# Performance work log

Measured on AMD Instinct MI355X. Metric: run time of the kernel, lower is better.

## Reference

```python
import jax, jax.numpy as jnp
import numpy as np

B, H, W, C = 8, 64, 64, 256
RC = C // 8  # reduced channels per build()

def setup_inputs() -> dict:
    key = jax.random.key(0)
    ks = jax.random.split(key, 4)
    x = jax.random.normal(ks[0], (B, H, W, C), dtype=jnp.float32)
    # 1x1 conv kernels flattened to [Cin, Cout]; glorot-ish scale
    wq = jax.random.normal(ks[1], (C, RC), dtype=jnp.float32) * (1.0 / np.sqrt(C))
    wk = jax.random.normal(ks[2], (C, RC), dtype=jnp.float32) * (1.0 / np.sqrt(C))
    wv = jax.random.normal(ks[3], (C, C), dtype=jnp.float32) * (1.0 / np.sqrt(C))
    bq = jnp.zeros((RC,), dtype=jnp.float32)
    bk = jnp.zeros((RC,), dtype=jnp.float32)
    bv = jnp.zeros((C,), dtype=jnp.float32)
    return {"x": x, "wq": wq, "bq": bq, "wk": wk, "bk": bk, "wv": wv, "bv": bv}

def reference(x, wq, bq, wk, bk, wv, bv):
    b, h, w, c = x.shape
    n = h * w
    # 1x1 convs == per-pixel channel matmuls; q/k have relu activation, v does not
    q = jax.nn.relu(jnp.einsum('bhwc,cd->bhwd', x, wq) + bq).reshape(b, n, -1)  # [B,N,RC]
    k = jax.nn.relu(jnp.einsum('bhwc,cd->bhwd', x, wk) + bk).reshape(b, n, -1)  # [B,N,RC]
    v = (jnp.einsum('bhwc,cd->bhwd', x, wv) + bv).reshape(b, n, c)              # [B,N,C]
    attn = jax.nn.softmax(jnp.einsum('bnd,bmd->bnm', q, k), axis=-1)            # [B,N,N]
    out = jnp.einsum('bnm,bmc->bnc', attn, v).reshape(b, h, w, c)
    return out + x
```

## Files before the change

kernel.cpp:

```cpp
#include <hip/hip_runtime.h>
#include <hip/hip_bf16.h>

typedef __attribute__((ext_vector_type(8))) short s16x8;
typedef __attribute__((ext_vector_type(4))) float f32x4;
typedef __attribute__((ext_vector_type(4))) unsigned int u32x4;

#define BATCH 8
#define NPIX  4096
#define CCH   256
#define RCH   32
#define TK    32
#define HALFK 2048
#define NIT   (HALFK / TK)
#define THR   8.0f
#define LOG2E 1.4426950408889634f

__device__ __forceinline__ unsigned short f2bf(float f) {
  __hip_bfloat16 h = __float2bfloat16(f);
  return __builtin_bit_cast(unsigned short, h);
}

__device__ __forceinline__ unsigned int cvt_pk(float lo, float hi) {
  unsigned int r;
  asm("v_cvt_pk_bf16_f32 %0, %1, %2" : "=v"(r) : "v"(lo), "v"(hi));
  return r;
}

__device__ __forceinline__ void gload_lds16(const void* g, void* l) {
  __builtin_amdgcn_global_load_lds(
      (const __attribute__((address_space(1))) void*)g,
      (__attribute__((address_space(3))) void*)l, 16, 0, 0);
}

__global__ void prep_kernel(const float* __restrict__ x,
                            const float* __restrict__ wq,
                            const float* __restrict__ wk,
                            const float* __restrict__ wv,
                            unsigned short* __restrict__ xb,
                            unsigned short* __restrict__ wqkT,
                            unsigned short* __restrict__ wvT) {
  int stride = gridDim.x * blockDim.x;
  int i0 = blockIdx.x * blockDim.x + threadIdx.x;
  const int nx4 = BATCH * NPIX * CCH / 4;
  for (int i = i0; i < nx4; i += stride) {
    float4 v = reinterpret_cast<const float4*>(x)[i];
    ushort4 o;
    o.x = f2bf(v.x); o.y = f2bf(v.y); o.z = f2bf(v.z); o.w = f2bf(v.w);
    reinterpret_cast<ushort4*>(xb)[i] = o;
  }
  for (int i = i0; i < 64 * CCH; i += stride) {
    int d = i >> 8, c = i & 255;
    float v = (d < RCH) ? wq[c * RCH + d] : wk[c * RCH + (d - RCH)];
    wqkT[i] = f2bf(v);
  }
  for (int i = i0; i < CCH * CCH; i += stride) {
    int d = i >> 8, c = i & 255;
    wvT[i] = f2bf(wv[c * CCH + d]);
  }
}

__global__ void proj_kernel(const unsigned short* __restrict__ xb,
                            const unsigned short* __restrict__ wqkT,
                            const unsigned short* __restrict__ wvT,
                            const float* __restrict__ bq,
                            const float* __restrict__ bk,
                            const float* __restrict__ bv,
                            unsigned short* __restrict__ qb,
                            unsigned short* __restrict__ kb,
                            unsigned short* __restrict__ vT) {
  int t = threadIdx.x;
  int w = t >> 6, l = t & 63, g = l >> 4, lc = l & 15;
  f32x4 zero = {0.f, 0.f, 0.f, 0.f};

  if (blockIdx.x < 512) {
    int row0 = blockIdx.x * 64 + w * 16;
    f32x4 acc[4];
    for (int ct = 0; ct < 4; ++ct) acc[ct] = zero;
    for (int ks = 0; ks < 8; ++ks) {
      s16x8 a = *reinterpret_cast<const s16x8*>(
          xb + (size_t)(row0 + lc) * CCH + ks * 32 + g * 8);
      for (int ct = 0; ct < 4; ++ct) {
        s16x8 bfr = *reinterpret_cast<const s16x8*>(
            wqkT + (size_t)(ct * 16 + lc) * CCH + ks * 32 + g * 8);
        acc[ct] = __builtin_amdgcn_mfma_f32_16x16x32_bf16(a, bfr, acc[ct], 0, 0, 0);
      }
    }
    for (int ct = 0; ct < 4; ++ct) {
      int col = ct * 16 + lc;
      float bias = (col < RCH) ? bq[col] : bk[col - RCH];
      for (int r = 0; r < 4; ++r) {
        int row = row0 + 4 * g + r;
        float v = fmaxf(acc[ct][r] + bias, 0.f);
        if (col < RCH) qb[(size_t)row * RCH + col] = f2bf(v * LOG2E);
        else           kb[(size_t)row * RCH + (col - RCH)] = f2bf(v);
      }
    }
  } else {
    int idx = blockIdx.x - 512;
    int b = idx & 7; idx >>= 3;
    int dt = idx & 3; int nt = idx >> 2;
    int d0 = dt * 64 + w * 16;
    int n0 = nt * 64;
    f32x4 acc[4];
    for (int ct = 0; ct < 4; ++ct) acc[ct] = zero;
    for (int ks = 0; ks < 8; ++ks) {
      s16x8 a = *reinterpret_cast<const s16x8*>(
          wvT + (size_t)(d0 + lc) * CCH + ks * 32 + g * 8);
      for (int ct = 0; ct < 4; ++ct) {
        s16x8 bfr = *reinterpret_cast<const s16x8*>(
            xb + ((size_t)b * NPIX + n0 + ct * 16 + lc) * CCH + ks * 32 + g * 8);
        acc[ct] = __builtin_amdgcn_mfma_f32_16x16x32_bf16(a, bfr, acc[ct], 0, 0, 0);
      }
    }
    for (int ct = 0; ct < 4; ++ct) {
      for (int r = 0; r < 4; ++r) {
        int d = d0 + 4 * g + r;
        int n = n0 + ct * 16 + lc;
        vT[((size_t)b * CCH + d) * NPIX + n] = f2bf(acc[ct][r] + bv[d]);
      }
    }
  }
}

__global__ __launch_bounds__(256, 2)
void attn_kernel(const unsigned short* __restrict__ qb,
                 const unsigned short* __restrict__ kb,
                 const unsigned short* __restrict__ vT,
                 const float* __restrict__ x,
                 float* __restrict__ out) {
  __shared__ __attribute__((aligned(16))) unsigned short Vlds[2][CCH * 64];
  __shared__ __attribute__((aligned(16))) float mergeLS[2][32];
  __shared__ float mLds[2];

  int b  = blockIdx.x & 7;
  int qt = blockIdx.x >> 3;
  int t  = threadIdx.x;
  int w = t >> 6, l = t & 63, g = l >> 4, lc = l & 15;
  int a = w >> 1, s = w & 1;
  const size_t bN = (size_t)b * NPIX;
  f32x4 zero = {0.f, 0.f, 0.f, 0.f};

  const unsigned short* kbase = kb + bN * RCH;
  const unsigned short* vbase = vT + (size_t)b * CCH * NPIX;

  int qbase = qt * 64 + a * 32;
  s16x8 qfA = *reinterpret_cast<const s16x8*>(qb + (bN + qbase + lc) * RCH + g * 8);
  s16x8 qfB = *reinterpret_cast<const s16x8*>(qb + (bN + qbase + 16 + lc) * RCH + g * 8);

  int chb = t >> 3, gr = t & 7;
  int gsw = gr ^ (chb & 7);
  int koff = (gsw < 4) ? (gsw * 8) : (HALFK + (gsw - 4) * 8);
  const unsigned short* vsrc = vbase + (size_t)chb * NPIX + koff;

  int krb = 8 * (lc >> 2) + (lc & 3);
  int kO  = s * HALFK + krb;

  unsigned int swz = (lc & 7) << 4;
  int vrS = (s * 64 + g * 16) ^ swz;

  s16x8 ones;
  #pragma unroll
  for (int i = 0; i < 8; ++i) ones[i] = (short)0x3F80;

  f32x4 o[2][16];
  #pragma unroll
  for (int qh = 0; qh < 2; ++qh)
    #pragma unroll
    for (int cc = 0; cc < 16; ++cc) o[qh][cc] = zero;
  f32x4 ols[2];
  ols[0] = zero; ols[1] = zero;
  float m = -1e30f;

  #pragma unroll
  for (int i = 0; i < 8; ++i)
    gload_lds16(vsrc + (size_t)i * 32 * NPIX,
                (char*)&Vlds[0][0] + i * 4096 + t * 16);
  s16x8 kf0 = *reinterpret_cast<const s16x8*>(kbase + (size_t)(kO + 0) * RCH + g * 8);
  s16x8 kf1 = *reinterpret_cast<const s16x8*>(kbase + (size_t)(kO + 4) * RCH + g * 8);
  __syncthreads();

  for (int it = 0; it < NIT; ++it) {
    int p = it & 1;
    int kv = it * TK;
    bool nx = (it + 1) < NIT;

    if (nx) {
      #pragma unroll
      for (int i = 0; i < 8; ++i)
        gload_lds16(vsrc + kv + TK + (size_t)i * 32 * NPIX,
                    (char*)&Vlds[p ^ 1][0] + i * 4096 + t * 16);
    }

    f32x4 sA0 = __builtin_amdgcn_mfma_f32_16x16x32_bf16(kf0, qfA, zero, 0, 0, 0);
    f32x4 sA1 = __builtin_amdgcn_mfma_f32_16x16x32_bf16(kf1, qfA, zero, 0, 0, 0);
    f32x4 sB0 = __builtin_amdgcn_mfma_f32_16x16x32_bf16(kf0, qfB, zero, 0, 0, 0);
    f32x4 sB1 = __builtin_amdgcn_mfma_f32_16x16x32_bf16(kf1, qfB, zero, 0, 0, 0);

    if (nx) {
      kf0 = *reinterpret_cast<const s16x8*>(
          kbase + (size_t)(kO + kv + TK + 0) * RCH + g * 8);
      kf1 = *reinterpret_cast<const s16x8*>(
          kbase + (size_t)(kO + kv + TK + 4) * RCH + g * 8);
    }

    float xA = fmaxf(fmaxf(sA0[0], sA0[1]), fmaxf(sA0[2], sA0[3]));
    float xB = fmaxf(fmaxf(sA1[0], sA1[1]), fmaxf(sA1[2], sA1[3]));
    float xC = fmaxf(fmaxf(sB0[0], sB0[1]), fmaxf(sB0[2], sB0[3]));
    float xD = fmaxf(fmaxf(sB1[0], sB1[1]), fmaxf(sB1[2], sB1[3]));
    float pmax = fmaxf(fmaxf(xA, xB), fmaxf(xC, xD));

    float sc = 1.f;
    int resc = !__all(pmax - m <= THR);
    if (resc) {
      #pragma unroll
      for (int off = 1; off <= 32; off <<= 1)
        pmax = fmaxf(pmax, __shfl_xor(pmax, off));
      float mnew = fmaxf(m, pmax);
      sc = exp2f(m - mnew);
      m = mnew;
    }

    unsigned int pkA[4], pkB[4];
    pkA[0] = cvt_pk(exp2f(sA0[0] - m), exp2f(sA0[1] - m));
    pkA[1] = cvt_pk(exp2f(sA0[2] - m), exp2f(sA0[3] - m));
    pkA[2] = cvt_pk(exp2f(sA1[0] - m), exp2f(sA1[1] - m));
    pkA[3] = cvt_pk(exp2f(sA1[2] - m), exp2f(sA1[3] - m));
    pkB[0] = cvt_pk(exp2f(sB0[0] - m), exp2f(sB0[1] - m));
    pkB[1] = cvt_pk(exp2f(sB0[2] - m), exp2f(sB0[3] - m));
    pkB[2] = cvt_pk(exp2f(sB1[0] - m), exp2f(sB1[1] - m));
    pkB[3] = cvt_pk(exp2f(sB1[2] - m), exp2f(sB1[3] - m));

    if (resc) {
      #pragma unroll
      for (int qh = 0; qh < 2; ++qh) {
        #pragma unroll
        for (int cc = 0; cc < 16; ++cc)
          #pragma unroll
          for (int r = 0; r < 4; ++r) o[qh][cc][r] *= sc;
        #pragma unroll
        for (int r = 0; r < 4; ++r) ols[qh][r] *= sc;
      }
    }

    u32x4 uA = {pkA[0], pkA[1], pkA[2], pkA[3]};
    u32x4 uB = {pkB[0], pkB[1], pkB[2], pkB[3]};
    s16x8 paA = __builtin_bit_cast(s16x8, uA);
    s16x8 paB = __builtin_bit_cast(s16x8, uB);
    const char* pb = (const char*)&Vlds[p][0] + lc * 128 + vrS;
    __builtin_amdgcn_s_setprio(1);
    ols[0] = __builtin_amdgcn_mfma_f32_16x16x32_bf16(paA, ones, ols[0], 0, 0, 0);
    ols[1] = __builtin_amdgcn_mfma_f32_16x16x32_bf16(paB, ones, ols[1], 0, 0, 0);
    #pragma unroll
    for (int cc = 0; cc < 16; ++cc) {
      s16x8 vb = *reinterpret_cast<const s16x8*>(pb + cc * 2048);
      o[0][cc] = __builtin_amdgcn_mfma_f32_16x16x32_bf16(paA, vb, o[0][cc], 0, 0, 0);
      o[1][cc] = __builtin_amdgcn_mfma_f32_16x16x32_bf16(paB, vb, o[1][cc], 0, 0, 0);
    }
    __builtin_amdgcn_s_setprio(0);

    __syncthreads();
  }

  if (s == 1) {
    if (lc == 0) {
      *reinterpret_cast<f32x4*>(&mergeLS[a][4 * g])      = ols[0];
      *reinterpret_cast<f32x4*>(&mergeLS[a][16 + 4 * g]) = ols[1];
    }
    if (l == 0) mLds[a] = m;
  }
  __syncthreads();

  float* mrg = (float*)&Vlds[0][0];
  if (s == 1) {
    float* base = mrg + a * 8192 + l * 128;
    #pragma unroll
    for (int qh = 0; qh < 2; ++qh)
      #pragma unroll
      for (int cc = 0; cc < 16; ++cc) {
        int idx = qh * 16 + cc;
        *reinterpret_cast<f32x4*>(base + ((idx + l) & 31) * 4) = o[qh][cc];
      }
  }
  __syncthreads();
  if (s == 0) {
    float mB = mLds[a];
    float mT = fmaxf(m, mB);
    float sAc = exp2f(m - mT), sBc = exp2f(mB - mT);
    const float* base = mrg + a * 8192 + l * 128;
    #pragma unroll
    for (int qh = 0; qh < 2; ++qh) {
      f32x4 lB4 = *reinterpret_cast<const f32x4*>(&mergeLS[a][qh * 16 + 4 * g]);
      f32x4 rl;
      #pragma unroll
      for (int r = 0; r < 4; ++r)
        rl[r] = 1.0f / (ols[qh][r] * sAc + lB4[r] * sBc);
      #pragma unroll
      for (int cc = 0; cc < 16; ++cc) {
        int idx = qh * 16 + cc;
        f32x4 ob = *reinterpret_cast<const f32x4*>(base + ((idx + l) & 31) * 4);
        #pragma unroll
        for (int r = 0; r < 4; ++r) {
          size_t row = bN + qbase + qh * 16 + 4 * g + r;
          size_t oi = row * CCH + cc * 16 + lc;
          out[oi] = (o[qh][cc][r] * sAc + ob[r] * sBc) * rl[r] + x[oi];
        }
      }
    }
  }
}

extern "C" void kernel_launch(void* const* d_in, const int* in_sizes, int n_in,
                              void* d_out, int out_size, void* d_ws, size_t ws_size,
                              hipStream_t stream) {
  const float* x  = (const float*)d_in[0];
  const float* wq = (const float*)d_in[1];
  const float* bq = (const float*)d_in[2];
  const float* wk = (const float*)d_in[3];
  const float* bk = (const float*)d_in[4];
  const float* wv = (const float*)d_in[5];
  const float* bv = (const float*)d_in[6];
  float* out = (float*)d_out;

  unsigned short* ws   = (unsigned short*)d_ws;
  unsigned short* qb   = ws;
  unsigned short* kb   = qb + 1048576;
  unsigned short* vT   = kb + 1048576;
  unsigned short* xb   = vT + 8388608;
  unsigned short* wqkT = xb + 8388608;
  unsigned short* wvT  = wqkT + 16384;

  prep_kernel<<<dim3(2048), dim3(256), 0, stream>>>(x, wq, wk, wv, xb, wqkT, wvT);
  proj_kernel<<<dim3(2560), dim3(256), 0, stream>>>(xb, wqkT, wvT, bq, bk, bv,
                                                    qb, kb, vT);
  attn_kernel<<<dim3(512), dim3(256), 0, stream>>>(qb, kb, vT, x, out);
}
```

Before: 164.4 us.

## Fuse x bf16 conversion into projection kernel via padded LDS tile

Removes the full-tensor fp32-to-bf16 conversion pass over x and its bf16 workspace. Each projection block now loads its 64-row fp32 slice of x, converts it to bf16 into a padded shared-memory tile, and feeds the MFMA operands from LDS. Weight prep stays as a small separate kernel. The trade-off is that the value-projection blocks re-read fp32 x four times instead of bf16, doubling the bytes of that redundant traffic.

```diff
diff --git a/kernel.cpp b/kernel.cpp
--- a/kernel.cpp
+++ b/kernel.cpp
@@ -14,6 +14,7 @@
 #define NIT   (HALFK / TK)
 #define THR   8.0f
 #define LOG2E 1.4426950408889634f
+#define XPAD  264
 
 __device__ __forceinline__ unsigned short f2bf(float f) {
   __hip_bfloat16 h = __float2bfloat16(f);
@@ -32,22 +33,13 @@
       (__attribute__((address_space(3))) void*)l, 16, 0, 0);
 }
 
-__global__ void prep_kernel(const float* __restrict__ x,
-                            const float* __restrict__ wq,
-                            const float* __restrict__ wk,
-                            const float* __restrict__ wv,
-                            unsigned short* __restrict__ xb,
-                            unsigned short* __restrict__ wqkT,
-                            unsigned short* __restrict__ wvT) {
+__global__ void wprep_kernel(const float* __restrict__ wq,
+                             const float* __restrict__ wk,
+                             const float* __restrict__ wv,
+                             unsigned short* __restrict__ wqkT,
+                             unsigned short* __restrict__ wvT) {
   int stride = gridDim.x * blockDim.x;
   int i0 = blockIdx.x * blockDim.x + threadIdx.x;
-  const int nx4 = BATCH * NPIX * CCH / 4;
-  for (int i = i0; i < nx4; i += stride) {
-    float4 v = reinterpret_cast<const float4*>(x)[i];
-    ushort4 o;
-    o.x = f2bf(v.x); o.y = f2bf(v.y); o.z = f2bf(v.z); o.w = f2bf(v.w);
-    reinterpret_cast<ushort4*>(xb)[i] = o;
-  }
   for (int i = i0; i < 64 * CCH; i += stride) {
     int d = i >> 8, c = i & 255;
     float v = (d < RCH) ? wq[c * RCH + d] : wk[c * RCH + (d - RCH)];
@@ -59,26 +51,41 @@
   }
 }
 
-__global__ void proj_kernel(const unsigned short* __restrict__ xb,
-                            const unsigned short* __restrict__ wqkT,
-                            const unsigned short* __restrict__ wvT,
-                            const float* __restrict__ bq,
-                            const float* __restrict__ bk,
-                            const float* __restrict__ bv,
-                            unsigned short* __restrict__ qb,
-                            unsigned short* __restrict__ kb,
-                            unsigned short* __restrict__ vT) {
+__global__ __launch_bounds__(256)
+void proj_kernel(const float* __restrict__ x,
+                 const unsigned short* __restrict__ wqkT,
+                 const unsigned short* __restrict__ wvT,
+                 const float* __restrict__ bq,
+                 const float* __restrict__ bk,
+                 const float* __restrict__ bv,
+                 unsigned short* __restrict__ qb,
+                 unsigned short* __restrict__ kb,
+                 unsigned short* __restrict__ vT) {
+  __shared__ __attribute__((aligned(16))) unsigned short Xt[64 * XPAD];
+
   int t = threadIdx.x;
   int w = t >> 6, l = t & 63, g = l >> 4, lc = l & 15;
   f32x4 zero = {0.f, 0.f, 0.f, 0.f};
 
   if (blockIdx.x < 512) {
-    int row0 = blockIdx.x * 64 + w * 16;
+    int row0 = blockIdx.x * 64;
+    #pragma unroll
+    for (int i = 0; i < 16; ++i) {
+      int flat4 = i * 256 + t;
+      int row = flat4 >> 6, col4 = flat4 & 63;
+      float4 v = *reinterpret_cast<const float4*>(
+          x + ((size_t)(row0 + row)) * CCH + col4 * 4);
+      ushort4 o4;
+      o4.x = f2bf(v.x); o4.y = f2bf(v.y); o4.z = f2bf(v.z); o4.w = f2bf(v.w);
+      *reinterpret_cast<ushort4*>(&Xt[row * XPAD + col4 * 4]) = o4;
+    }
+    __syncthreads();
+
     f32x4 acc[4];
     for (int ct = 0; ct < 4; ++ct) acc[ct] = zero;
     for (int ks = 0; ks < 8; ++ks) {
       s16x8 a = *reinterpret_cast<const s16x8*>(
-          xb + (size_t)(row0 + lc) * CCH + ks * 32 + g * 8);
+          &Xt[(w * 16 + lc) * XPAD + ks * 32 + g * 8]);
       for (int ct = 0; ct < 4; ++ct) {
         s16x8 bfr = *reinterpret_cast<const s16x8*>(
             wqkT + (size_t)(ct * 16 + lc) * CCH + ks * 32 + g * 8);
@@ -89,7 +96,7 @@
       int col = ct * 16 + lc;
       float bias = (col < RCH) ? bq[col] : bk[col - RCH];
       for (int r = 0; r < 4; ++r) {
-        int row = row0 + 4 * g + r;
+        int row = row0 + w * 16 + 4 * g + r;
         float v = fmaxf(acc[ct][r] + bias, 0.f);
         if (col < RCH) qb[(size_t)row * RCH + col] = f2bf(v * LOG2E);
         else           kb[(size_t)row * RCH + (col - RCH)] = f2bf(v);
@@ -101,6 +108,18 @@
     int dt = idx & 3; int nt = idx >> 2;
     int d0 = dt * 64 + w * 16;
     int n0 = nt * 64;
+    #pragma unroll
+    for (int i = 0; i < 16; ++i) {
+      int flat4 = i * 256 + t;
+      int row = flat4 >> 6, col4 = flat4 & 63;
+      float4 v = *reinterpret_cast<const float4*>(
+          x + ((size_t)b * NPIX + n0 + row) * CCH + col4 * 4);
+      ushort4 o4;
+      o4.x = f2bf(v.x); o4.y = f2bf(v.y); o4.z = f2bf(v.z); o4.w = f2bf(v.w);
+      *reinterpret_cast<ushort4*>(&Xt[row * XPAD + col4 * 4]) = o4;
+    }
+    __syncthreads();
+
     f32x4 acc[4];
     for (int ct = 0; ct < 4; ++ct) acc[ct] = zero;
     for (int ks = 0; ks < 8; ++ks) {
@@ -108,7 +127,7 @@
           wvT + (size_t)(d0 + lc) * CCH + ks * 32 + g * 8);
       for (int ct = 0; ct < 4; ++ct) {
         s16x8 bfr = *reinterpret_cast<const s16x8*>(
-            xb + ((size_t)b * NPIX + n0 + ct * 16 + lc) * CCH + ks * 32 + g * 8);
+            &Xt[(ct * 16 + lc) * XPAD + ks * 32 + g * 8]);
         acc[ct] = __builtin_amdgcn_mfma_f32_16x16x32_bf16(a, bfr, acc[ct], 0, 0, 0);
       }
     }
@@ -325,12 +344,11 @@
   unsigned short* qb   = ws;
   unsigned short* kb   = qb + 1048576;
   unsigned short* vT   = kb + 1048576;
-  unsigned short* xb   = vT + 8388608;
-  unsigned short* wqkT = xb + 8388608;
+  unsigned short* wqkT = vT + 8388608;
   unsigned short* wvT  = wqkT + 16384;
 
-  prep_kernel<<<dim3(2048), dim3(256), 0, stream>>>(x, wq, wk, wv, xb, wqkT, wvT);
-  proj_kernel<<<dim3(2560), dim3(256), 0, stream>>>(xb, wqkT, wvT, bq, bk, bv,
+  wprep_kernel<<<dim3(80), dim3(256), 0, stream>>>(wq, wk, wv, wqkT, wvT);
+  proj_kernel<<<dim3(2560), dim3(256), 0, stream>>>(x, wqkT, wvT, bq, bk, bv,
                                                     qb, kb, vT);
   attn_kernel<<<dim3(512), dim3(256), 0, stream>>>(qb, kb, vT, x, out);
 }
```

Measured after the change: 139.8 us (median of 2 runs). 15.0% less time.
